# Kernel optimization log

Measured on AMD Instinct MI355X. Metric: run time of the kernel, lower is better.

Reference implementation:

```python
import jax, jax.numpy as jnp
import numpy as np

MARGIN = 1.0
EPS = 1e-6
DIAG_BIG = 99999.0


def setup_inputs() -> dict:
    key = jax.random.key(0)
    x = jax.random.normal(key, (16384, 256), dtype=jnp.float32)
    # HardNet descriptors are unit-L2 normalized (the distance formula assumes it)
    x = x / jnp.linalg.norm(x, axis=1, keepdims=True)
    return {"x": x}


def reference(x) -> jnp.ndarray:
    cnt = x.shape[0] // 2
    a = x[:cnt]          # [N, d] anchors
    p = x[cnt:]          # [N, d] positives
    # pairwise unit-L2 distance: sqrt((1 - a.p^T + eps) * 2)
    dmat = jnp.sqrt((1.0 - jnp.matmul(a, p.T) + EPS) * 2.0)  # [N, N]
    pos = jnp.diagonal(dmat)                                  # [N]
    # mask diagonal with large constant, then row/col mins = hard negatives
    masked = dmat + jnp.eye(cnt, dtype=dmat.dtype) * DIAG_BIG
    min_a = jnp.min(masked, axis=0)   # best negative anchor per positive
    min_p = jnp.min(masked, axis=1)   # best negative positive per anchor
    neg = jnp.minimum(min_a, min_p)   # [N]
    return jnp.mean(jnp.clip(MARGIN - neg + pos, 0.0))
```

## Files before the change

kernel.cpp:

```cpp
#include <hip/hip_runtime.h>


#define CNT   8192
#define KDIM  256
#define BIGF  3.0e38f

typedef __bf16 bf16x8 __attribute__((ext_vector_type(8)));
typedef float  f32x4  __attribute__((ext_vector_type(4)));

__device__ __forceinline__ unsigned short f2bf(float f) {
    unsigned u = __float_as_uint(f);
    u += 0x7FFFu + ((u >> 16) & 1u);
    return (unsigned short)(u >> 16);
}

__device__ __forceinline__ void async16(const void* g, void* l) {
    __builtin_amdgcn_global_load_lds(
        (const __attribute__((address_space(1))) unsigned int*)g,
        (__attribute__((address_space(3))) unsigned int*)l,
        16, 0, 0);
}


__global__ __launch_bounds__(256) void convert_init_kernel(
    const float* __restrict__ x, unsigned short* __restrict__ xb,
    unsigned* __restrict__ mins)
{
    int t = blockIdx.x * 256 + threadIdx.x;
    int elem = t * 8;
    int row  = elem >> 8;
    int col  = elem & 255;
    int q    = (col >> 3) & 7;
    int qs   = q ^ (row & 7);
    float4 v0 = *(const float4*)(x + elem);
    float4 v1 = *(const float4*)(x + elem + 4);
    uint4 w;
    w.x = (unsigned)f2bf(v0.x) | ((unsigned)f2bf(v0.y) << 16);
    w.y = (unsigned)f2bf(v0.z) | ((unsigned)f2bf(v0.w) << 16);
    w.z = (unsigned)f2bf(v1.x) | ((unsigned)f2bf(v1.y) << 16);
    w.w = (unsigned)f2bf(v1.z) | ((unsigned)f2bf(v1.w) << 16);
    *(uint4*)(xb + (row << 8) + (col & ~63) + qs * 8) = w;
    if (t < 2 * CNT) mins[t] = 0x7F7FFFFFu;
}

#define TST 132
__global__ __launch_bounds__(256, 2) void dist3_kernel(
    const unsigned short* __restrict__ Ab, const unsigned short* __restrict__ Pb,
    unsigned* __restrict__ g_rowmin, unsigned* __restrict__ g_colmin,
    float* __restrict__ g_pos)
{
    __shared__ unsigned short As[128 * 64];
    __shared__ unsigned short Bs[256 * 64];
    float* T = (float*)Bs;

    const int tid  = threadIdx.x;
    const int l    = blockIdx.x;
    const int xcd  = l & 7;
    const int i    = l >> 3;
    const int bm   = (xcd >> 1) * 16 + (i & 15);
    const int bn   = (xcd & 1) * 16 + (i >> 4);

    const int wave = tid >> 6;
    const int lane = tid & 63;
    const int quad = lane >> 4;
    const int l15  = lane & 15;
    const int wm   = wave >> 1;
    const int wn   = wave & 1;

    f32x4 acc[4][8];
    #pragma unroll
    for (int a = 0; a < 4; a++)
        #pragma unroll
        for (int b = 0; b < 8; b++)
            acc[a][b] = (f32x4){0.f, 0.f, 0.f, 0.f};

    int a_off[4][2], b_off[8][2];
    #pragma unroll
    for (int mi = 0; mi < 4; mi++) {
        int ra = wm * 64 + mi * 16 + l15;
        #pragma unroll
        for (int ks = 0; ks < 2; ks++)
            a_off[mi][ks] = ra * 128 + (((ks * 4 + quad) ^ (ra & 7)) * 16);
    }
    #pragma unroll
    for (int ni = 0; ni < 8; ni++) {
        int rb = wn * 128 + ni * 16 + l15;
        #pragma unroll
        for (int ks = 0; ks < 2; ks++)
            b_off[ni][ks] = rb * 128 + (((ks * 4 + quad) ^ (rb & 7)) * 16);
    }

    const int srow8 = lane >> 3;
    const int sq    = lane & 7;

    #pragma unroll
    for (int kc = 0; kc < 4; kc++) {
        #pragma unroll
        for (int g = 0; g < 4; g++) {
            int r0 = wave * 32 + g * 8;
            async16(Ab + (size_t)(bm * 128 + r0 + srow8) * 256 + kc * 64 + sq * 8,
                    &As[r0 * 64]);
        }
        #pragma unroll
        for (int g = 0; g < 8; g++) {
            int r0 = wave * 64 + g * 8;
            async16(Pb + (size_t)(bn * 256 + r0 + srow8) * 256 + kc * 64 + sq * 8,
                    &Bs[r0 * 64]);
        }
        __syncthreads();
        #pragma unroll
        for (int ks = 0; ks < 2; ks++) {
            bf16x8 af[4], bfr[8];
            #pragma unroll
            for (int mi = 0; mi < 4; mi++)
                af[mi] = *(const bf16x8*)((const char*)As + a_off[mi][ks]);
            #pragma unroll
            for (int ni = 0; ni < 8; ni++)
                bfr[ni] = *(const bf16x8*)((const char*)Bs + b_off[ni][ks]);
            #pragma unroll
            for (int mi = 0; mi < 4; mi++)
                #pragma unroll
                for (int ni = 0; ni < 8; ni++)
                    acc[mi][ni] = __builtin_amdgcn_mfma_f32_16x16x32_bf16(
                        af[mi], bfr[ni], acc[mi][ni], 0, 0, 0);
        }
        __syncthreads();
    }


    if ((bm >> 1) == bn) {
        const int dstart = (bm & 1) * 128;
        #pragma unroll
        for (int mi = 0; mi < 4; mi++)
            #pragma unroll
            for (int ni = 0; ni < 8; ni++)
                #pragma unroll
                for (int r = 0; r < 4; r++) {
                    int rl = wm * 64 + mi * 16 + quad * 4 + r;
                    int cl = wn * 128 + ni * 16 + l15;
                    if (cl == rl + dstart) {
                        g_pos[bm * 128 + rl] = (1.0f - acc[mi][ni][r] + 1e-6f) * 2.0f;
                        acc[mi][ni][r] = -BIGF;
                    }
                }
    }

    #pragma unroll
    for (int ni = 0; ni < 8; ni++) {
        float v = -BIGF;
        #pragma unroll
        for (int mi = 0; mi < 4; mi++)
            #pragma unroll
            for (int r = 0; r < 4; r++)
                v = fmaxf(v, acc[mi][ni][r]);
        v = fmaxf(v, __shfl_xor(v, 16, 64));
        v = fmaxf(v, __shfl_xor(v, 32, 64));
        if (quad == 0) {
            float tt = fmaxf((1.0f - v + 1e-6f) * 2.0f, 0.0f);
            atomicMin(&g_colmin[bn * 256 + wn * 128 + ni * 16 + l15],
                      __float_as_uint(tt));
        }
    }

    float rmax[4][4];
    #pragma unroll
    for (int mi = 0; mi < 4; mi++)
        #pragma unroll
        for (int r = 0; r < 4; r++) {
            float v = acc[mi][0][r];
            #pragma unroll
            for (int ni = 1; ni < 8; ni++) v = fmaxf(v, acc[mi][ni][r]);
            rmax[mi][r] = v;
        }
    __syncthreads();
    const int centry = wn * 16 + l15;
    #pragma unroll
    for (int mi = 0; mi < 4; mi++) {
        f32x4 v = {rmax[mi][0], rmax[mi][1], rmax[mi][2], rmax[mi][3]};
        *(f32x4*)&T[centry * TST + wm * 64 + mi * 16 + quad * 4] = v;
    }
    __syncthreads();

    if (tid < 128) {
        int row = tid;
        float v0 = T[row], v1 = T[TST + row];
        #pragma unroll
        for (int c = 2; c < 32; c += 2) {
            v0 = fmaxf(v0, T[c * TST + row]);
            v1 = fmaxf(v1, T[(c + 1) * TST + row]);
        }
        float v = fmaxf(v0, v1);
        float tt = fmaxf((1.0f - v + 1e-6f) * 2.0f, 0.0f);
        atomicMin(&g_rowmin[bm * 128 + row], __float_as_uint(tt));
    }
}

__global__ __launch_bounds__(1024) void finalize_t_kernel(
    const unsigned* __restrict__ rm, const unsigned* __restrict__ cm,
    const float* __restrict__ post, float* __restrict__ out)
{
    float local = 0.f;
    for (int i = threadIdx.x; i < CNT; i += 1024) {
        float t   = fminf(__uint_as_float(rm[i]), __uint_as_float(cm[i]));
        float neg = sqrtf(fmaxf(t, 0.f));
        float pos = sqrtf(fmaxf(post[i], 0.f));
        local += fmaxf(1.0f - neg + pos, 0.0f);
    }
    #pragma unroll
    for (int m = 1; m < 64; m <<= 1) local += __shfl_xor(local, m, 64);
    __shared__ float wsum[16];
    if ((threadIdx.x & 63) == 0) wsum[threadIdx.x >> 6] = local;
    __syncthreads();
    if (threadIdx.x == 0) {
        float s = 0.f;
        #pragma unroll
        for (int w = 0; w < 16; w++) s += wsum[w];
        out[0] = s * (1.0f / (float)CNT);
    }
}


#define BM 128
#define BN 128
#define BK 64
#define KST (BK + 8)

__global__ __launch_bounds__(256) void init_min_kernel(unsigned* buf, int n) {
    int i = blockIdx.x * 256 + threadIdx.x;
    if (i < n) buf[i] = 0x7F7FFFFFu;
}

__global__ __launch_bounds__(256) void dist_tile_kernel(
    const float* __restrict__ A, const float* __restrict__ P,
    unsigned* __restrict__ g_rowmin, unsigned* __restrict__ g_colmin,
    float* __restrict__ g_pos)
{
    __shared__ unsigned short As[BM * KST];
    __shared__ unsigned short Bs[BN * KST];
    __shared__ unsigned redrow[BM];
    __shared__ unsigned redcol[BN];

    const int tid  = threadIdx.x;
    const int bm   = blockIdx.y;
    const int bn   = blockIdx.x;
    const int wave = tid >> 6;
    const int lane = tid & 63;
    const int quad = lane >> 4;
    const int l15  = lane & 15;
    const int m_off = (wave >> 1) * 64;
    const int n_off = (wave & 1) * 64;

    if (tid < BM) redrow[tid] = 0x7F7FFFFFu;
    if (tid < BN) redcol[tid] = 0x7F7FFFFFu;

    f32x4 acc[4][4];
    #pragma unroll
    for (int i = 0; i < 4; i++)
        #pragma unroll
        for (int j = 0; j < 4; j++)
            acc[i][j] = (f32x4){0.f, 0.f, 0.f, 0.f};

    const int srow = tid >> 4;
    const int scol = tid & 15;

    for (int kc = 0; kc < KDIM / BK; kc++) {
        #pragma unroll
        for (int i = 0; i < 8; i++) {
            int r = srow + i * 16;
            float4 va = *(const float4*)(A + (size_t)(bm * BM + r) * KDIM + kc * BK + scol * 4);
            float4 vb = *(const float4*)(P + (size_t)(bn * BN + r) * KDIM + kc * BK + scol * 4);
            ushort4 wa, wb;
            wa.x = f2bf(va.x); wa.y = f2bf(va.y); wa.z = f2bf(va.z); wa.w = f2bf(va.w);
            wb.x = f2bf(vb.x); wb.y = f2bf(vb.y); wb.z = f2bf(vb.z); wb.w = f2bf(vb.w);
            *(ushort4*)(&As[r * KST + scol * 4]) = wa;
            *(ushort4*)(&Bs[r * KST + scol * 4]) = wb;
        }
        __syncthreads();
        #pragma unroll
        for (int ks = 0; ks < BK / 32; ks++) {
            bf16x8 af[4], bfr[4];
            #pragma unroll
            for (int mi = 0; mi < 4; mi++)
                af[mi] = *(const bf16x8*)(&As[(m_off + mi * 16 + l15) * KST + ks * 32 + quad * 8]);
            #pragma unroll
            for (int ni = 0; ni < 4; ni++)
                bfr[ni] = *(const bf16x8*)(&Bs[(n_off + ni * 16 + l15) * KST + ks * 32 + quad * 8]);
            #pragma unroll
            for (int mi = 0; mi < 4; mi++)
                #pragma unroll
                for (int ni = 0; ni < 4; ni++)
                    acc[mi][ni] = __builtin_amdgcn_mfma_f32_16x16x32_bf16(
                        af[mi], bfr[ni], acc[mi][ni], 0, 0, 0);
        }
        __syncthreads();
    }

    float rmin[4][4], cmin[4];
    #pragma unroll
    for (int mi = 0; mi < 4; mi++)
        #pragma unroll
        for (int r = 0; r < 4; r++) rmin[mi][r] = BIGF;
    #pragma unroll
    for (int ni = 0; ni < 4; ni++) cmin[ni] = BIGF;

    const int grow0 = bm * BM + m_off + quad * 4;
    const int gcol0 = bn * BN + n_off + l15;

    #pragma unroll
    for (int mi = 0; mi < 4; mi++)
        #pragma unroll
        for (int ni = 0; ni < 4; ni++) {
            int gcol = gcol0 + ni * 16;
            #pragma unroll
            for (int r = 0; r < 4; r++) {
                int grow = grow0 + mi * 16 + r;
                float s = acc[mi][ni][r];
                float d = sqrtf((1.0f - s + 1e-6f) * 2.0f);
                float dm = d;
                if (grow == gcol) { g_pos[grow] = d; dm = BIGF; }
                rmin[mi][r] = fminf(rmin[mi][r], dm);
                cmin[ni]    = fminf(cmin[ni], dm);
            }
        }

    #pragma unroll
    for (int mi = 0; mi < 4; mi++)
        #pragma unroll
        for (int r = 0; r < 4; r++) {
            float v = rmin[mi][r];
            v = fminf(v, __shfl_xor(v, 1, 64));
            v = fminf(v, __shfl_xor(v, 2, 64));
            v = fminf(v, __shfl_xor(v, 4, 64));
            v = fminf(v, __shfl_xor(v, 8, 64));
            rmin[mi][r] = v;
        }
    #pragma unroll
    for (int ni = 0; ni < 4; ni++) {
        float v = cmin[ni];
        v = fminf(v, __shfl_xor(v, 16, 64));
        v = fminf(v, __shfl_xor(v, 32, 64));
        cmin[ni] = v;
    }

    if (l15 == 0) {
        #pragma unroll
        for (int mi = 0; mi < 4; mi++)
            #pragma unroll
            for (int r = 0; r < 4; r++)
                atomicMin(&redrow[m_off + mi * 16 + quad * 4 + r],
                          __float_as_uint(rmin[mi][r]));
    }
    if (quad == 0) {
        #pragma unroll
        for (int ni = 0; ni < 4; ni++)
            atomicMin(&redcol[n_off + ni * 16 + l15], __float_as_uint(cmin[ni]));
    }
    __syncthreads();

    if (tid < 128) atomicMin(&g_rowmin[bm * BM + tid], redrow[tid]);
    else           atomicMin(&g_colmin[bn * BN + (tid - 128)], redcol[tid - 128]);
}

__global__ __launch_bounds__(1024) void finalize_kernel(
    const unsigned* __restrict__ g_rowmin, const unsigned* __restrict__ g_colmin,
    const float* __restrict__ g_pos, float* __restrict__ out)
{
    float local = 0.f;
    for (int i = threadIdx.x; i < CNT; i += 1024) {
        float neg = fminf(__uint_as_float(g_rowmin[i]), __uint_as_float(g_colmin[i]));
        float v = 1.0f - neg + g_pos[i];
        local += fmaxf(v, 0.0f);
    }
    #pragma unroll
    for (int m = 1; m < 64; m <<= 1) local += __shfl_xor(local, m, 64);
    __shared__ float wsum[16];
    if ((threadIdx.x & 63) == 0) wsum[threadIdx.x >> 6] = local;
    __syncthreads();
    if (threadIdx.x == 0) {
        float s = 0.f;
        #pragma unroll
        for (int w = 0; w < 16; w++) s += wsum[w];
        out[0] = s * (1.0f / (float)CNT);
    }
}


extern "C" void kernel_launch(void* const* d_in, const int* in_sizes, int n_in,
                              void* d_out, int out_size, void* d_ws, size_t ws_size,
                              hipStream_t stream) {
    const float* x = (const float*)d_in[0];
    float* out = (float*)d_out;

    const size_t bf16_bytes = (size_t)2 * CNT * KDIM * 2;
    const size_t need = bf16_bytes + (size_t)2 * CNT * 4 + (size_t)CNT * 4;

    if (ws_size >= need) {
        unsigned short* xb   = (unsigned short*)d_ws;
        unsigned*       mins = (unsigned*)((char*)d_ws + bf16_bytes);
        float*          pos  = (float*)(mins + 2 * CNT);
        convert_init_kernel<<<dim3(2048), dim3(256), 0, stream>>>(x, xb, mins);
        dist3_kernel<<<dim3(2048), dim3(256), 0, stream>>>(
            xb, xb + (size_t)CNT * KDIM, mins, mins + CNT, pos);
        finalize_t_kernel<<<dim3(1), dim3(1024), 0, stream>>>(mins, mins + CNT, pos, out);
    } else {
        unsigned* rowmin = (unsigned*)d_ws;
        unsigned* colmin = rowmin + CNT;
        float*    pos    = (float*)(colmin + CNT);
        init_min_kernel<<<dim3(2 * CNT / 256), dim3(256), 0, stream>>>(rowmin, 2 * CNT);
        dist_tile_kernel<<<dim3(CNT / BN, CNT / BM), dim3(256), 0, stream>>>(
            x, x + (size_t)CNT * KDIM, rowmin, colmin, pos);
        finalize_kernel<<<dim3(1), dim3(1024), 0, stream>>>(rowmin, colmin, pos, out);
    }
}
```

Baseline: 106.0 us.

## Load MFMA operands directly from global memory, dropping LDS staging

Removes the async global-to-LDS staging of A and B tiles along with the swizzled bf16 layout. Each wave now reads its bf16x8 fragments straight from global memory (via L1/L2) for all 8 k-steps, and shared memory is kept only for the row-max transpose buffer. This drops the LDS round trip and the per-chunk barriers, but loads that were shared within a block are now repeated by each wave in global memory. It also reads the row-major layout in an uncoalesced, row-strided pattern, which may raise cache traffic.

```diff
diff --git a/kernel.cpp b/kernel.cpp
--- a/kernel.cpp
+++ b/kernel.cpp
@@ -14,13 +14,6 @@
     return (unsigned short)(u >> 16);
 }
 
-__device__ __forceinline__ void async16(const void* g, void* l) {
-    __builtin_amdgcn_global_load_lds(
-        (const __attribute__((address_space(1))) unsigned int*)g,
-        (__attribute__((address_space(3))) unsigned int*)l,
-        16, 0, 0);
-}
-
 
 __global__ __launch_bounds__(256) void convert_init_kernel(
     const float* __restrict__ x, unsigned short* __restrict__ xb,
@@ -28,10 +21,6 @@
 {
     int t = blockIdx.x * 256 + threadIdx.x;
     int elem = t * 8;
-    int row  = elem >> 8;
-    int col  = elem & 255;
-    int q    = (col >> 3) & 7;
-    int qs   = q ^ (row & 7);
     float4 v0 = *(const float4*)(x + elem);
     float4 v1 = *(const float4*)(x + elem + 4);
     uint4 w;
@@ -39,19 +28,17 @@
     w.y = (unsigned)f2bf(v0.z) | ((unsigned)f2bf(v0.w) << 16);
     w.z = (unsigned)f2bf(v1.x) | ((unsigned)f2bf(v1.y) << 16);
     w.w = (unsigned)f2bf(v1.z) | ((unsigned)f2bf(v1.w) << 16);
-    *(uint4*)(xb + (row << 8) + (col & ~63) + qs * 8) = w;
+    *(uint4*)(xb + elem) = w;
     if (t < 2 * CNT) mins[t] = 0x7F7FFFFFu;
 }
 
 #define TST 132
-__global__ __launch_bounds__(256, 2) void dist3_kernel(
+__global__ __launch_bounds__(256, 2) void dist4_kernel(
     const unsigned short* __restrict__ Ab, const unsigned short* __restrict__ Pb,
     unsigned* __restrict__ g_rowmin, unsigned* __restrict__ g_colmin,
     float* __restrict__ g_pos)
 {
-    __shared__ unsigned short As[128 * 64];
-    __shared__ unsigned short Bs[256 * 64];
-    float* T = (float*)Bs;
+    __shared__ float T[32 * TST];
 
     const int tid  = threadIdx.x;
     const int l    = blockIdx.x;
@@ -74,57 +61,31 @@
         for (int b = 0; b < 8; b++)
             acc[a][b] = (f32x4){0.f, 0.f, 0.f, 0.f};
 
-    int a_off[4][2], b_off[8][2];
-    #pragma unroll
-    for (int mi = 0; mi < 4; mi++) {
-        int ra = wm * 64 + mi * 16 + l15;
-        #pragma unroll
-        for (int ks = 0; ks < 2; ks++)
-            a_off[mi][ks] = ra * 128 + (((ks * 4 + quad) ^ (ra & 7)) * 16);
-    }
-    #pragma unroll
-    for (int ni = 0; ni < 8; ni++) {
-        int rb = wn * 128 + ni * 16 + l15;
-        #pragma unroll
-        for (int ks = 0; ks < 2; ks++)
-            b_off[ni][ks] = rb * 128 + (((ks * 4 + quad) ^ (rb & 7)) * 16);
-    }
-
-    const int srow8 = lane >> 3;
-    const int sq    = lane & 7;
-
-    #pragma unroll
-    for (int kc = 0; kc < 4; kc++) {
-        #pragma unroll
-        for (int g = 0; g < 4; g++) {
-            int r0 = wave * 32 + g * 8;
-            async16(Ab + (size_t)(bm * 128 + r0 + srow8) * 256 + kc * 64 + sq * 8,
-                    &As[r0 * 64]);
-        }
-        #pragma unroll
-        for (int g = 0; g < 8; g++) {
-            int r0 = wave * 64 + g * 8;
-            async16(Pb + (size_t)(bn * 256 + r0 + srow8) * 256 + kc * 64 + sq * 8,
-                    &Bs[r0 * 64]);
-        }
-        __syncthreads();
-        #pragma unroll
-        for (int ks = 0; ks < 2; ks++) {
-            bf16x8 af[4], bfr[8];
-            #pragma unroll
-            for (int mi = 0; mi < 4; mi++)
-                af[mi] = *(const bf16x8*)((const char*)As + a_off[mi][ks]);
+    const char* Abase = (const char*)Ab;
+    const char* Pbase = (const char*)Pb;
+    size_t a_off[4], b_off[8];
+    #pragma unroll
+    for (int mi = 0; mi < 4; mi++)
+        a_off[mi] = ((size_t)(bm * 128 + wm * 64 + mi * 16 + l15) << 9) + quad * 16;
+    #pragma unroll
+    for (int ni = 0; ni < 8; ni++)
+        b_off[ni] = ((size_t)(bn * 256 + wn * 128 + ni * 16 + l15) << 9) + quad * 16;
+
+    #pragma unroll
+    for (int ks = 0; ks < 8; ks++) {
+        bf16x8 af[4], bfr[8];
+        #pragma unroll
+        for (int mi = 0; mi < 4; mi++)
+            af[mi] = *(const bf16x8*)(Abase + a_off[mi] + ks * 64);
+        #pragma unroll
+        for (int ni = 0; ni < 8; ni++)
+            bfr[ni] = *(const bf16x8*)(Pbase + b_off[ni] + ks * 64);
+        #pragma unroll
+        for (int mi = 0; mi < 4; mi++)
             #pragma unroll
             for (int ni = 0; ni < 8; ni++)
-                bfr[ni] = *(const bf16x8*)((const char*)Bs + b_off[ni][ks]);
-            #pragma unroll
-            for (int mi = 0; mi < 4; mi++)
-                #pragma unroll
-                for (int ni = 0; ni < 8; ni++)
-                    acc[mi][ni] = __builtin_amdgcn_mfma_f32_16x16x32_bf16(
-                        af[mi], bfr[ni], acc[mi][ni], 0, 0, 0);
-        }
-        __syncthreads();
+                acc[mi][ni] = __builtin_amdgcn_mfma_f32_16x16x32_bf16(
+                    af[mi], bfr[ni], acc[mi][ni], 0, 0, 0);
     }
 
 
@@ -172,7 +133,6 @@
             for (int ni = 1; ni < 8; ni++) v = fmaxf(v, acc[mi][ni][r]);
             rmax[mi][r] = v;
         }
-    __syncthreads();
     const int centry = wn * 16 + l15;
     #pragma unroll
     for (int mi = 0; mi < 4; mi++) {
@@ -399,7 +359,7 @@
         unsigned*       mins = (unsigned*)((char*)d_ws + bf16_bytes);
         float*          pos  = (float*)(mins + 2 * CNT);
         convert_init_kernel<<<dim3(2048), dim3(256), 0, stream>>>(x, xb, mins);
-        dist3_kernel<<<dim3(2048), dim3(256), 0, stream>>>(
+        dist4_kernel<<<dim3(2048), dim3(256), 0, stream>>>(
             xb, xb + (size_t)CNT * KDIM, mins, mins + CNT, pos);
         finalize_t_kernel<<<dim3(1), dim3(1024), 0, stream>>>(mins, mins + CNT, pos, out);
     } else {
```

Measured after the change: 169.5 us. 59.9% more time.
